# Performance work log

Hardware: AMD Instinct MI355X
Metric: run time of the kernel (lower is better)

Reference implementation:

```python
import jax, jax.numpy as jnp
import numpy as np

N_LINKS = 262144
N_PAIRS = 4194304
F = 20   # feature_size
R = 20   # readout_units
T = 4    # message passing iterations


def setup_inputs() -> dict:
    key = jax.random.key(0)
    ks = jax.random.split(key, 16)
    s = 0.1
    return {
        "link_state": jax.random.normal(ks[0], (N_LINKS, F), dtype=jnp.float32),
        "first": jax.random.randint(ks[1], (N_PAIRS,), 0, N_LINKS),
        "second": jax.random.randint(ks[2], (N_PAIRS,), 0, N_LINKS),
        "state_dim": F,
        # message MLP: Linear(2F -> F)
        "W_msg": jax.random.normal(ks[3], (F, 2 * F), dtype=jnp.float32) * s,
        "b_msg": jnp.zeros((F,), dtype=jnp.float32),
        # GRUCell params (PyTorch layout: [3F, in] with r,z,n gate order)
        "W_ih": jax.random.normal(ks[4], (3 * F, F), dtype=jnp.float32) * s,
        "W_hh": jax.random.normal(ks[5], (3 * F, F), dtype=jnp.float32) * s,
        "b_ih": jnp.zeros((3 * F,), dtype=jnp.float32),
        "b_hh": jnp.zeros((3 * F,), dtype=jnp.float32),
        # readout: Linear(F->R) SELU, Linear(R->R) SELU
        "W_r1": jax.random.normal(ks[6], (R, F), dtype=jnp.float32) * s,
        "b_r1": jnp.zeros((R,), dtype=jnp.float32),
        "W_r2": jax.random.normal(ks[7], (R, R), dtype=jnp.float32) * s,
        "b_r2": jnp.zeros((R,), dtype=jnp.float32),
        # out layer: Linear(R->1)
        "W_out": jax.random.normal(ks[8], (1, R), dtype=jnp.float32) * s,
        "b_out": jnp.zeros((1,), dtype=jnp.float32),
    }


def _gru_cell(m, h, W_ih, W_hh, b_ih, b_hh):
    # PyTorch GRUCell math, gate order (r, z, n)
    gi = m @ W_ih.T + b_ih   # [N, 3F]
    gh = h @ W_hh.T + b_hh   # [N, 3F]
    i_r, i_z, i_n = jnp.split(gi, 3, axis=1)
    h_r, h_z, h_n = jnp.split(gh, 3, axis=1)
    r = jax.nn.sigmoid(i_r + h_r)
    z = jax.nn.sigmoid(i_z + h_z)
    n = jnp.tanh(i_n + r * h_n)
    return (1.0 - z) * n + z * h


def reference(link_state, first, second, state_dim,
              W_msg, b_msg, W_ih, W_hh, b_ih, b_hh,
              W_r1, b_r1, W_r2, b_r2, W_out, b_out):
    state = link_state  # [N_LINKS, F]
    for _ in range(T):
        main_edges = state[first]    # gather [N_PAIRS, F]
        neigh_edges = state[second]  # gather [N_PAIRS, F]
        edges_concat = jnp.concatenate([main_edges, neigh_edges], axis=1)
        m = jax.nn.selu(edges_concat @ W_msg.T + b_msg)  # [N_PAIRS, F]
        agg = jnp.zeros_like(state).at[second].add(m)    # scatter_add back to links
        state = _gru_cell(agg, state, W_ih, W_hh, b_ih, b_hh)
    feature = jnp.sum(state, axis=0)  # [F]
    h1 = jax.nn.selu(W_r1 @ feature + b_r1)
    h2 = jax.nn.selu(W_r2 @ h1 + b_r2)
    return W_out @ h2 + b_out  # [1]
```

## Files before the change

kernel.cpp:

```cpp
#include <hip/hip_runtime.h>
#include <hip/hip_fp16.h>

#define N_LINKS 262144
#define N_PAIRS 4194304
#define F 20
#define XB 20
#define T_ITERS 4

#define NSB 256
#define LPS 1024
#define PB 128
#define PT 1024
#define PCHUNK (N_PAIRS / PB)
#define PPT (PCHUNK / PT)

typedef float f32x2 __attribute__((ext_vector_type(2)));
typedef _Float16 h16x2 __attribute__((ext_vector_type(2)));

__device__ __forceinline__ float selu_f(float x) {
    const float scale = 1.0507009873554805f;
    const float scale_alpha = 1.7580993408473766f;
    return x > 0.0f ? scale * x : scale_alpha * (__expf(x) - 1.0f);
}

__device__ __forceinline__ float selu_b(float x) {
    const float s = 1.0507009873554805f;
    const float sa = 1.7580993408473766f;
    const float mx = fmaxf(x, 0.0f);
    const float mn = fminf(x, 0.0f);
    return fmaf(sa, __expf(mn), fmaf(s, mx, -sa));
}

__device__ __forceinline__ float sigmoid_f(float x) {
    return 1.0f / (1.0f + __expf(-x));
}

__device__ __forceinline__ float tanh_fast(float x) {
    x = fminf(fmaxf(x, -15.0f), 15.0f);
    float e = __expf(2.0f * x);
    return (e - 1.0f) / (e + 1.0f);
}

__device__ __forceinline__ void store_row_fp8(unsigned char* rowp, const float* o1) {
    int* p = (int*)rowp;
#pragma unroll
    for (int i = 0; i < 5; ++i) {
        int w = 0;
        w = __builtin_amdgcn_cvt_pk_fp8_f32(o1[4*i+0], o1[4*i+1], w, false);
        w = __builtin_amdgcn_cvt_pk_fp8_f32(o1[4*i+2], o1[4*i+3], w, true);
        p[i] = w;
    }
}


__global__ void __launch_bounds__(PT)
k_part(const int* __restrict__ first, const int* __restrict__ second,
       int* __restrict__ ent, int* __restrict__ ptable, int* __restrict__ sectot) {
    __shared__ int hist[NSB];
    __shared__ int cur[NSB];
    const int b = blockIdx.x;
    const int cbase = b * PCHUNK;
    const int tid = threadIdx.x;
    for (int i = tid; i < NSB; i += PT) hist[i] = 0;
    __syncthreads();
    int sv[PPT];
#pragma unroll
    for (int k = 0; k < PPT; ++k) {
        sv[k] = second[cbase + k * PT + tid];
        atomicAdd(&hist[sv[k] >> 10], 1);
    }
    __syncthreads();
    if (tid < NSB) {
        int acc = 0;
        for (int j = 0; j < tid; ++j) acc += hist[j];
        cur[tid] = acc;
        ptable[b * (NSB + 1) + tid] = acc;
        if (tid == 0) ptable[b * (NSB + 1) + NSB] = PCHUNK;
        atomicAdd(&sectot[tid], hist[tid]);
    }
    __syncthreads();
#pragma unroll
    for (int k = 0; k < PPT; ++k) {
        const int s = sv[k];
        const int f = first[cbase + k * PT + tid];
        const int pos = atomicAdd(&cur[s >> 10], 1);
        ent[cbase + pos] = f | ((s & 1023) << 18);
    }
}

__global__ void k_scan256(const int* __restrict__ sectot, int* __restrict__ sbase,
                          int* __restrict__ rs) {
    __shared__ int s[NSB];
    const int t = threadIdx.x;
    s[t] = sectot[t];
    __syncthreads();
    if (t == 0) {
        int acc = 0;
        for (int j = 0; j < NSB; ++j) { int c = s[j]; s[j] = acc; acc += c; }
    }
    __syncthreads();
    sbase[t] = s[t];
    if (t == 0) { sbase[NSB] = N_PAIRS; rs[N_LINKS] = N_PAIRS; }
}

__global__ void __launch_bounds__(PT)
k_build(const int* __restrict__ ptable, const int* __restrict__ sbase,
        const int* __restrict__ ent, int* __restrict__ srcs, int* __restrict__ rs) {
    __shared__ int rstart[PB];
    __shared__ int rlen[PB];
    __shared__ int lcnt[LPS];
    __shared__ int lown[LPS];
    __shared__ int cur[LPS];
    const int sb = blockIdx.x;
    const int tid = threadIdx.x;
    if (tid < PB) {
        const int o0 = ptable[tid * (NSB + 1) + sb];
        const int o1 = ptable[tid * (NSB + 1) + sb + 1];
        rstart[tid] = tid * PCHUNK + o0;
        rlen[tid] = o1 - o0;
    }
    lcnt[tid] = 0;
    __syncthreads();
    const int wave = tid >> 6;
    const int lane = tid & 63;
    for (int j = wave; j < PB; j += (PT >> 6)) {
        const int r0 = rstart[j], rl = rlen[j];
        for (int i = lane; i < rl; i += 64)
            atomicAdd(&lcnt[(ent[r0 + i] >> 18) & 1023], 1);
    }
    __syncthreads();
    const int own = lcnt[tid];
    lown[tid] = own;
    for (int off = 1; off < LPS; off <<= 1) {
        const int v = (tid >= off) ? lcnt[tid - off] : 0;
        __syncthreads();
        lcnt[tid] += v;
        __syncthreads();
    }
    const int sbb = sbase[sb];
    const int excl = lcnt[tid] - lown[tid];
    rs[sb * LPS + tid] = sbb + excl;
    cur[tid] = excl;
    __syncthreads();
    for (int j = wave; j < PB; j += (PT >> 6)) {
        const int r0 = rstart[j], rl = rlen[j];
        for (int i = lane; i < rl; i += 64) {
            const int e = ent[r0 + i];
            const int pos = atomicAdd(&cur[(e >> 18) & 1023], 1);
            srcs[sbb + pos] = (e & 0x3FFFF) * 20;
        }
    }
}


__global__ void k_premsg(const float* __restrict__ state,
                         const float* __restrict__ W_msg,
                         const float* __restrict__ b_msg,
                         unsigned char* __restrict__ X1b, __half* __restrict__ X2h) {
    __shared__ float Wl[F * 2 * F];
    __shared__ float bl[F];
    for (int i = threadIdx.x; i < F * 2 * F; i += blockDim.x) Wl[i] = W_msg[i];
    if (threadIdx.x < F) bl[threadIdx.x] = b_msg[threadIdx.x];
    __syncthreads();

    int l = blockIdx.x * blockDim.x + threadIdx.x;

    float s[F];
    const float4* sp = (const float4*)(state + (size_t)l * F);
#pragma unroll
    for (int i = 0; i < 5; ++i) {
        float4 v = sp[i];
        s[4*i+0] = v.x; s[4*i+1] = v.y; s[4*i+2] = v.z; s[4*i+3] = v.w;
    }
    float o1[F], o2[F];
#pragma unroll
    for (int o = 0; o < F; ++o) {
        float a1 = bl[o], a2 = 0.0f;
#pragma unroll
        for (int k = 0; k < F; ++k) {
            a1 = fmaf(Wl[o * 2 * F + k],     s[k], a1);
            a2 = fmaf(Wl[o * 2 * F + F + k], s[k], a2);
        }
        o1[o] = a1; o2[o] = a2;
    }
    store_row_fp8(X1b + (size_t)l * XB, o1);
    __half2* xp = (__half2*)(X2h + (size_t)l * F);
#pragma unroll
    for (int i = 0; i < 10; ++i)
        xp[i] = __halves2half2(__float2half(o2[2*i]), __float2half(o2[2*i+1]));
}

__global__ void __launch_bounds__(256)
k_agg(const int* __restrict__ rs, const int* __restrict__ srcs,
      const unsigned char* __restrict__ X1b, const __half* __restrict__ X2h,
      float* __restrict__ agg) {
    const int wave = threadIdx.x >> 6;
    const int lane = threadIdx.x & 63;
    const int g = lane / 10;
    const int j = lane - g * 10;
    const int lb = (blockIdx.x * 4 + wave) * 6;

    const int link = lb + g;
    const bool active = (g < 6) && (link < N_LINKS);
    const int lclamp = active ? link : (N_LINKS - 1);
    const int row_start = rs[lclamp];
    const int cnt = active ? (rs[lclamp + 1] - row_start) : 0;
    const int cl = (cnt > 0) ? (cnt - 1) : 0;

    const __half2 hv = *(const __half2*)(X2h + (size_t)lclamp * F + 2 * j);
    const float x2a = __half2float(__low2half(hv));
    const float x2b = __half2float(__high2half(hv));

    int cmax = cnt;
#pragma unroll
    for (int off = 1; off < 64; off <<= 1)
        cmax = max(cmax, __shfl_xor(cmax, off, 64));

    const int gsel = (g < 6) ? g : 5;
    float acc_a = 0.0f, acc_b = 0.0f;

    for (int base = 0; base < cmax; base += 10) {
        const int sv = srcs[row_start + min(base + j, cl)];
#pragma unroll
        for (int r = 0; r < 10; ++r) {
            const int src = __shfl(sv, gsel * 10 + r, 64);
            const unsigned v = *(const unsigned short*)(X1b + src + 2 * j);
            const f32x2 xx = __builtin_amdgcn_cvt_pk_f32_fp8((int)v, false);
            const bool ok = (base + r) < cnt;
            acc_a += ok ? selu_b(xx[0] + x2a) : 0.0f;
            acc_b += ok ? selu_b(xx[1] + x2b) : 0.0f;
        }
    }
    if (active) {
        float2 o; o.x = acc_a; o.y = acc_b;
        *(float2*)(agg + (size_t)link * F + 2 * j) = o;
    }
}

__global__ void __launch_bounds__(256)
k_gru(const float* __restrict__ agg, const float* __restrict__ h_in,
      const float* __restrict__ W_ih, const float* __restrict__ W_hh,
      const float* __restrict__ b_ih, const float* __restrict__ b_hh,
      const float* __restrict__ W_msg, const float* __restrict__ b_msg,
      float* __restrict__ h_out, unsigned char* __restrict__ X1b,
      __half* __restrict__ X2h, float* __restrict__ feature, int flags) {
    __shared__ h16x2 WiH[3 * F * 10];
    __shared__ h16x2 WhH[3 * F * 10];
    __shared__ h16x2 WmH[F * 20];
    __shared__ float bi[3 * F];
    __shared__ float bh[3 * F];
    __shared__ float bm[F];
    __shared__ float red[4 * F];
    {
        _Float16* wi = (_Float16*)WiH;
        _Float16* wh = (_Float16*)WhH;
        for (int i = threadIdx.x; i < 3 * F * F; i += blockDim.x) {
            wi[i] = (_Float16)W_ih[i];
            wh[i] = (_Float16)W_hh[i];
        }
        _Float16* wm = (_Float16*)WmH;
        for (int i = threadIdx.x; i < F * 2 * F; i += blockDim.x)
            wm[i] = (_Float16)W_msg[i];
    }
    if (threadIdx.x < 3 * F) {
        bi[threadIdx.x] = b_ih[threadIdx.x];
        bh[threadIdx.x] = b_hh[threadIdx.x];
    }
    if (threadIdx.x < F) bm[threadIdx.x] = b_msg[threadIdx.x];
    __syncthreads();

    const int l = blockIdx.x * blockDim.x + threadIdx.x;

    float m[F], h[F];
    const float4* mp = (const float4*)(agg  + (size_t)l * F);
    const float4* hp = (const float4*)(h_in + (size_t)l * F);
#pragma unroll
    for (int i = 0; i < 5; ++i) {
        float4 vm = mp[i], vh = hp[i];
        m[4*i+0] = vm.x; m[4*i+1] = vm.y; m[4*i+2] = vm.z; m[4*i+3] = vm.w;
        h[4*i+0] = vh.x; h[4*i+1] = vh.y; h[4*i+2] = vh.z; h[4*i+3] = vh.w;
    }
    h16x2 mh[10], hh[10];
#pragma unroll
    for (int i = 0; i < 10; ++i) {
        mh[i][0] = (_Float16)m[2*i]; mh[i][1] = (_Float16)m[2*i+1];
        hh[i][0] = (_Float16)h[2*i]; hh[i][1] = (_Float16)h[2*i+1];
    }

    float hn[F];
#pragma unroll
    for (int j = 0; j < F; ++j) {
        float gri = 0.f, gzi = 0.f, gin = bi[2*F + j];
        float grh = 0.f, gzh = 0.f, ghn = bh[2*F + j];
#pragma unroll
        for (int k = 0; k < 10; ++k) {
            gri = __builtin_amdgcn_fdot2(WiH[(0*F + j) * 10 + k], mh[k], gri, false);
            gzi = __builtin_amdgcn_fdot2(WiH[(1*F + j) * 10 + k], mh[k], gzi, false);
            gin = __builtin_amdgcn_fdot2(WiH[(2*F + j) * 10 + k], mh[k], gin, false);
            grh = __builtin_amdgcn_fdot2(WhH[(0*F + j) * 10 + k], hh[k], grh, false);
            gzh = __builtin_amdgcn_fdot2(WhH[(1*F + j) * 10 + k], hh[k], gzh, false);
            ghn = __builtin_amdgcn_fdot2(WhH[(2*F + j) * 10 + k], hh[k], ghn, false);
        }
        float r = sigmoid_f(bi[j] + bh[j] + gri + grh);
        float z = sigmoid_f(bi[F + j] + bh[F + j] + gzi + gzh);
        float n = tanh_fast(gin + r * ghn);
        hn[j] = (1.0f - z) * n + z * h[j];
    }

    float4* op = (float4*)(h_out + (size_t)l * F);
#pragma unroll
    for (int i = 0; i < 5; ++i)
        op[i] = make_float4(hn[4*i], hn[4*i+1], hn[4*i+2], hn[4*i+3]);

    if (flags & 1) {
        h16x2 hnh[10];
#pragma unroll
        for (int i = 0; i < 10; ++i) {
            hnh[i][0] = (_Float16)hn[2*i]; hnh[i][1] = (_Float16)hn[2*i+1];
        }
        float o1[F], o2[F];
#pragma unroll
        for (int o = 0; o < F; ++o) {
            float a1 = bm[o], a2 = 0.0f;
#pragma unroll
            for (int k = 0; k < 10; ++k) {
                a1 = __builtin_amdgcn_fdot2(WmH[o * 20 + k],      hnh[k], a1, false);
                a2 = __builtin_amdgcn_fdot2(WmH[o * 20 + 10 + k], hnh[k], a2, false);
            }
            o1[o] = a1; o2[o] = a2;
        }
        store_row_fp8(X1b + (size_t)l * XB, o1);
        __half2* xp = (__half2*)(X2h + (size_t)l * F);
#pragma unroll
        for (int i = 0; i < 10; ++i)
            xp[i] = __halves2half2(__float2half(o2[2*i]), __float2half(o2[2*i+1]));
    }

    if (flags & 2) {
#pragma unroll
        for (int off = 1; off < 64; off <<= 1) {
#pragma unroll
            for (int j = 0; j < F; ++j) hn[j] += __shfl_xor(hn[j], off, 64);
        }
        const int lane = threadIdx.x & 63;
        const int wave = threadIdx.x >> 6;
        if (lane == 0) {
#pragma unroll
            for (int j = 0; j < F; ++j) red[wave * F + j] = hn[j];
        }
        __syncthreads();
        if (threadIdx.x < F) {
            float s = red[threadIdx.x] + red[F + threadIdx.x] +
                      red[2 * F + threadIdx.x] + red[3 * F + threadIdx.x];
            atomicAdd(&feature[threadIdx.x], s);
        }
    }
}

__global__ void k_readout(const float* __restrict__ feature,
                          const float* __restrict__ W_r1, const float* __restrict__ b_r1,
                          const float* __restrict__ W_r2, const float* __restrict__ b_r2,
                          const float* __restrict__ W_out, const float* __restrict__ b_out,
                          float* __restrict__ out) {
    if (threadIdx.x != 0 || blockIdx.x != 0) return;
    float fv[F], h1[F], h2[F];
#pragma unroll
    for (int i = 0; i < F; ++i) fv[i] = feature[i];
#pragma unroll
    for (int o = 0; o < F; ++o) {
        float a = b_r1[o];
#pragma unroll
        for (int k = 0; k < F; ++k) a = fmaf(W_r1[o * F + k], fv[k], a);
        h1[o] = selu_f(a);
    }
#pragma unroll
    for (int o = 0; o < F; ++o) {
        float a = b_r2[o];
#pragma unroll
        for (int k = 0; k < F; ++k) a = fmaf(W_r2[o * F + k], h1[k], a);
        h2[o] = selu_f(a);
    }
    float a = b_out[0];
#pragma unroll
    for (int k = 0; k < F; ++k) a = fmaf(W_out[k], h2[k], a);
    out[0] = a;
}

extern "C" void kernel_launch(void* const* d_in, const int* in_sizes, int n_in,
                              void* d_out, int out_size, void* d_ws, size_t ws_size,
                              hipStream_t stream) {
    const float* link_state = (const float*)d_in[0];
    const int*   first      = (const int*)  d_in[1];
    const int*   second     = (const int*)  d_in[2];
    const float* W_msg = (const float*)d_in[4];
    const float* b_msg = (const float*)d_in[5];
    const float* W_ih  = (const float*)d_in[6];
    const float* W_hh  = (const float*)d_in[7];
    const float* b_ih  = (const float*)d_in[8];
    const float* b_hh  = (const float*)d_in[9];
    const float* W_r1  = (const float*)d_in[10];
    const float* b_r1  = (const float*)d_in[11];
    const float* W_r2  = (const float*)d_in[12];
    const float* b_r2  = (const float*)d_in[13];
    const float* W_out = (const float*)d_in[14];
    const float* b_out = (const float*)d_in[15];
    float* out = (float*)d_out;

    const size_t NF = (size_t)N_LINKS * F;
    float* state   = (float*)d_ws;
    float* agg     = state + NF;
    unsigned char* X1b = (unsigned char*)(agg + NF);
    __half* X2h    = (__half*)(X1b + (size_t)N_LINKS * XB + 64);
    int*    srcs   = (int*)(X2h + NF);
    int*    rs     = srcs + N_PAIRS;
    float* feature = (float*)(rs + N_LINKS + 1);
    int* ptable    = (int*)(feature + 32);
    int* sectot    = ptable + PB * (NSB + 1);
    int* sbase     = sectot + NSB;
    int* ent       = (int*)agg;

    hipMemsetAsync(sectot, 0, NSB * sizeof(int), stream);
    hipMemsetAsync(feature, 0, F * sizeof(float), stream);

    k_part<<<PB, PT, 0, stream>>>(first, second, ent, ptable, sectot);
    k_scan256<<<1, NSB, 0, stream>>>(sectot, sbase, rs);
    k_build<<<NSB, PT, 0, stream>>>(ptable, sbase, ent, srcs, rs);

    k_premsg<<<N_LINKS / 256, 256, 0, stream>>>(link_state, W_msg, b_msg, X1b, X2h);
    const int aggBlocks = (N_LINKS + 23) / 24;
    for (int t = 0; t < T_ITERS; ++t) {
        const float* h = (t == 0) ? link_state : state;
        int flags = (t < T_ITERS - 1 ? 1 : 0) | (t == T_ITERS - 1 ? 2 : 0);
        k_agg<<<aggBlocks, 256, 0, stream>>>(rs, srcs, X1b, X2h, agg);
        k_gru<<<N_LINKS / 256, 256, 0, stream>>>(agg, h, W_ih, W_hh, b_ih, b_hh,
                                                 W_msg, b_msg, state, X1b, X2h,
                                                 feature, flags);
    }
    k_readout<<<1, 64, 0, stream>>>(feature, W_r1, b_r1, W_r2, b_r2, W_out, b_out, out);
}
```

Before: 626.8 us.

## Sort links by in-degree inside each super-block to balance aggregation waves

```diff
diff --git a/kernel.cpp b/kernel.cpp
--- a/kernel.cpp
+++ b/kernel.cpp
@@ -9,7 +9,7 @@
 
 #define NSB 256
 #define LPS 1024
-#define PB 128
+#define PB 256
 #define PT 1024
 #define PCHUNK (N_PAIRS / PB)
 #define PPT (PCHUNK / PT)
@@ -105,12 +105,15 @@
 
 __global__ void __launch_bounds__(PT)
 k_build(const int* __restrict__ ptable, const int* __restrict__ sbase,
-        const int* __restrict__ ent, int* __restrict__ srcs, int* __restrict__ rs) {
+        const int* __restrict__ ent, int* __restrict__ srcs, int* __restrict__ rs,
+        int* __restrict__ lid) {
     __shared__ int rstart[PB];
     __shared__ int rlen[PB];
     __shared__ int lcnt[LPS];
-    __shared__ int lown[LPS];
     __shared__ int cur[LPS];
+    __shared__ int dhist[64];
+    __shared__ int dbase[64];
+    __shared__ int dcur[64];
     const int sb = blockIdx.x;
     const int tid = threadIdx.x;
     if (tid < PB) {
@@ -120,6 +123,7 @@
         rlen[tid] = o1 - o0;
     }
     lcnt[tid] = 0;
+    if (tid < 64) { dhist[tid] = 0; dcur[tid] = 0; }
     __syncthreads();
     const int wave = tid >> 6;
     const int lane = tid & 63;
@@ -129,8 +133,19 @@
             atomicAdd(&lcnt[(ent[r0 + i] >> 18) & 1023], 1);
     }
     __syncthreads();
-    const int own = lcnt[tid];
-    lown[tid] = own;
+    const int count = lcnt[tid];
+    const int dbin = min(count, 63);
+    atomicAdd(&dhist[dbin], 1);
+    __syncthreads();
+    if (tid == 0) {
+        int acc = 0;
+        for (int b = 0; b < 64; ++b) { dbase[b] = acc; acc += dhist[b]; }
+    }
+    __syncthreads();
+    const int rank = dbase[dbin] + atomicAdd(&dcur[dbin], 1);
+    lcnt[rank] = count;
+    lid[sb * LPS + rank] = sb * LPS + tid;
+    __syncthreads();
     for (int off = 1; off < LPS; off <<= 1) {
         const int v = (tid >= off) ? lcnt[tid - off] : 0;
         __syncthreads();
@@ -138,8 +153,8 @@
         __syncthreads();
     }
     const int sbb = sbase[sb];
-    const int excl = lcnt[tid] - lown[tid];
-    rs[sb * LPS + tid] = sbb + excl;
+    const int excl = lcnt[rank] - count;
+    rs[sb * LPS + rank] = sbb + excl;
     cur[tid] = excl;
     __syncthreads();
     for (int j = wave; j < PB; j += (PT >> 6)) {
@@ -191,23 +206,25 @@
 }
 
 __global__ void __launch_bounds__(256)
-k_agg(const int* __restrict__ rs, const int* __restrict__ srcs,
+k_agg(const int* __restrict__ rs, const int* __restrict__ lid,
+      const int* __restrict__ srcs,
       const unsigned char* __restrict__ X1b, const __half* __restrict__ X2h,
       float* __restrict__ agg) {
     const int wave = threadIdx.x >> 6;
     const int lane = threadIdx.x & 63;
     const int g = lane / 10;
     const int j = lane - g * 10;
-    const int lb = (blockIdx.x * 4 + wave) * 6;
-
-    const int link = lb + g;
-    const bool active = (g < 6) && (link < N_LINKS);
-    const int lclamp = active ? link : (N_LINKS - 1);
-    const int row_start = rs[lclamp];
-    const int cnt = active ? (rs[lclamp + 1] - row_start) : 0;
+    const int gsel = (g < 6) ? g : 5;
+    const int slot = (blockIdx.x * 4 + wave) * 6 + gsel;
+
+    const bool active = (g < 6) && (slot < N_LINKS);
+    const int sc = min(slot, N_LINKS - 1);
+    const int link = lid[sc];
+    const int row_start = rs[sc];
+    const int cnt = active ? (rs[sc + 1] - row_start) : 0;
     const int cl = (cnt > 0) ? (cnt - 1) : 0;
 
-    const __half2 hv = *(const __half2*)(X2h + (size_t)lclamp * F + 2 * j);
+    const __half2 hv = *(const __half2*)(X2h + (size_t)link * F + 2 * j);
     const float x2a = __half2float(__low2half(hv));
     const float x2b = __half2float(__high2half(hv));
 
@@ -216,7 +233,6 @@
     for (int off = 1; off < 64; off <<= 1)
         cmax = max(cmax, __shfl_xor(cmax, off, 64));
 
-    const int gsel = (g < 6) ? g : 5;
     float acc_a = 0.0f, acc_b = 0.0f;
 
     for (int base = 0; base < cmax; base += 10) {
@@ -413,7 +429,8 @@
     __half* X2h    = (__half*)(X1b + (size_t)N_LINKS * XB + 64);
     int*    srcs   = (int*)(X2h + NF);
     int*    rs     = srcs + N_PAIRS;
-    float* feature = (float*)(rs + N_LINKS + 1);
+    int*    lid    = rs + N_LINKS + 1;
+    float* feature = (float*)(lid + N_LINKS);
     int* ptable    = (int*)(feature + 32);
     int* sectot    = ptable + PB * (NSB + 1);
     int* sbase     = sectot + NSB;
@@ -424,14 +441,14 @@
 
     k_part<<<PB, PT, 0, stream>>>(first, second, ent, ptable, sectot);
     k_scan256<<<1, NSB, 0, stream>>>(sectot, sbase, rs);
-    k_build<<<NSB, PT, 0, stream>>>(ptable, sbase, ent, srcs, rs);
+    k_build<<<NSB, PT, 0, stream>>>(ptable, sbase, ent, srcs, rs, lid);
 
     k_premsg<<<N_LINKS / 256, 256, 0, stream>>>(link_state, W_msg, b_msg, X1b, X2h);
     const int aggBlocks = (N_LINKS + 23) / 24;
     for (int t = 0; t < T_ITERS; ++t) {
         const float* h = (t == 0) ? link_state : state;
         int flags = (t < T_ITERS - 1 ? 1 : 0) | (t == T_ITERS - 1 ? 2 : 0);
-        k_agg<<<aggBlocks, 256, 0, stream>>>(rs, srcs, X1b, X2h, agg);
+        k_agg<<<aggBlocks, 256, 0, stream>>>(rs, lid, srcs, X1b, X2h, agg);
         k_gru<<<N_LINKS / 256, 256, 0, stream>>>(agg, h, W_ih, W_hh, b_ih, b_hh,
                                                  W_msg, b_msg, state, X1b, X2h,
                                                  feature, flags);
```

Measured after the change: 584.9 us, median of 2. 6.7% less time.
